# Kernel optimization log

Measured on AMD Instinct MI355X. Metric: run time of the kernel, lower is better.

Reference implementation:

```python
import jax, jax.numpy as jnp
import numpy as np

B, S, H, DIN, DOUT = 4, 2048, 8, 128, 128


def setup_inputs() -> dict:
    key = jax.random.key(0)
    ks = jax.random.split(key, 11)
    sc = 0.05
    return {
        "q": jax.random.normal(ks[0], (B, S, DIN), jnp.float32),
        "k": jax.random.normal(ks[1], (B, S, DIN), jnp.float32),
        "v": jax.random.normal(ks[2], (B, S, DOUT), jnp.float32),
        "Wq": jax.random.normal(ks[3], (DIN, DIN * H), jnp.float32) * sc,
        "bq": jax.random.normal(ks[4], (DIN * H,), jnp.float32) * sc,
        "Wk": jax.random.normal(ks[5], (DIN, DIN * H), jnp.float32) * sc,
        "bk": jax.random.normal(ks[6], (DIN * H,), jnp.float32) * sc,
        "Wv": jax.random.normal(ks[7], (DOUT, DOUT * H), jnp.float32) * sc,
        "bv": jax.random.normal(ks[8], (DOUT * H,), jnp.float32) * sc,
        "Wo": jax.random.normal(ks[9], (H * DOUT, DOUT), jnp.float32) * sc,
        "bo": jax.random.normal(ks[10], (DOUT,), jnp.float32) * sc,
    }


def reference(q, k, v, Wq, bq, Wk, bk, Wv, bv, Wo, bo):
    b, s, din = q.shape
    dout = v.shape[-1]
    h = Wq.shape[1] // din
    # project and split heads: [B, S, H, D] -> [B, H, S, D]
    qs = (q @ Wq + bq).reshape(b, s, h, din).transpose(0, 2, 1, 3)
    kh = (k @ Wk + bk).reshape(b, k.shape[1], h, din).transpose(0, 2, 1, 3)
    vh = (v @ Wv + bv).reshape(b, v.shape[1], h, dout).transpose(0, 2, 1, 3)
    # scaled dot-product attention; note the original scales by sqrt(input_dim)
    scale = 1.0 / jnp.sqrt(jnp.asarray(din, q.dtype))
    scores = jnp.einsum("bhqd,bhkd->bhqk", qs, kh) * scale
    attn = jax.nn.softmax(scores, axis=-1)
    out = jnp.einsum("bhqk,bhkd->bhqd", attn, vh)  # [B, H, S, Dout]
    out = out.transpose(0, 2, 1, 3).reshape(b, s, h * dout)
    return out @ Wo + bo
```

## Files before the change

### kernel.cpp

```cpp
#include <hip/hip_runtime.h>
#include <hip/hip_bf16.h>
#include <stdint.h>

typedef __bf16 bf16_t;
typedef bf16_t bf16x8 __attribute__((ext_vector_type(8)));
typedef bf16_t bf16x4 __attribute__((ext_vector_type(4)));
typedef float  f32x4  __attribute__((ext_vector_type(4)));

#define MFMA_BF16 __builtin_amdgcn_mfma_f32_16x16x32_bf16

constexpr int BB = 4, SS = 2048, HH = 8;
constexpr float QK_SCALE = 0.08838834764831845f;

__device__ __forceinline__ void dma16(const bf16_t* g, bf16_t* l) {
    __builtin_amdgcn_global_load_lds(
        (const __attribute__((address_space(1))) void*)g,
        (__attribute__((address_space(3))) void*)l, 16, 0, 0);
}

__global__ void prep_weights(const float* __restrict__ Wq, const float* __restrict__ Wk,
                             const float* __restrict__ Wv, const float* __restrict__ Wo,
                             bf16_t* __restrict__ WqT, bf16_t* __restrict__ WkT,
                             bf16_t* __restrict__ WvT, bf16_t* __restrict__ WoT)
{
    __shared__ float tile[64][65];
    int bid = blockIdx.x;
    int m = bid >> 5, tl = bid & 31;
    const float* src; bf16_t* dst; int R, C, tr, tc; float scale = 1.0f;
    if (m < 3) {
        src = (m == 0) ? Wq : (m == 1) ? Wk : Wv;
        dst = (m == 0) ? WqT : (m == 1) ? WkT : WvT;
        R = 128; C = 1024; tr = tl >> 4; tc = tl & 15;
        if (m == 0) scale = QK_SCALE;
    } else {
        src = Wo; dst = WoT; R = 1024; C = 128; tr = tl >> 1; tc = tl & 1;
    }
    int r0 = tr * 64, c0 = tc * 64;
    int t = threadIdx.x, rr = t >> 2, cc = (t & 3) * 16;
    const float4* s4 = (const float4*)(src + (size_t)(r0 + rr) * C + c0 + cc);
    #pragma unroll
    for (int i = 0; i < 4; ++i) {
        float4 f = s4[i];
        tile[rr][cc + 4 * i + 0] = f.x; tile[rr][cc + 4 * i + 1] = f.y;
        tile[rr][cc + 4 * i + 2] = f.z; tile[rr][cc + 4 * i + 3] = f.w;
    }
    __syncthreads();
    bf16x8 o0, o1;
    #pragma unroll
    for (int i = 0; i < 8; ++i) o0[i] = (bf16_t)(tile[cc + i][rr] * scale);
    #pragma unroll
    for (int i = 0; i < 8; ++i) o1[i] = (bf16_t)(tile[cc + 8 + i][rr] * scale);
    bf16_t* d = dst + (size_t)(c0 + rr) * R + r0 + cc;
    *(bf16x8*)d = o0;
    *(bf16x8*)(d + 8) = o1;
}

__global__ __launch_bounds__(256, 2)
void proj_kernel(const float* __restrict__ qin, const float* __restrict__ kin,
                 const float* __restrict__ vin,
                 const bf16_t* __restrict__ WqT, const bf16_t* __restrict__ WkT,
                 const bf16_t* __restrict__ WvT,
                 const float* __restrict__ bq, const float* __restrict__ bk,
                 const float* __restrict__ bv,
                 bf16_t* __restrict__ Qh, bf16_t* __restrict__ Kh, bf16_t* __restrict__ VhT)
{
    __shared__ __align__(16) bf16_t a_lds[128][136];
    __shared__ __align__(16) bf16_t b_lds[128][136];
    const int z = blockIdx.z;
    const float*  A    = (z == 0) ? qin : (z == 1) ? kin : vin;
    const bf16_t* BT   = (z == 0) ? WqT : (z == 1) ? WkT : WvT;
    const float*  bias = (z == 0) ? bq  : (z == 1) ? bk  : bv;
    bf16_t*       out  = (z == 0) ? Qh  : (z == 1) ? Kh  : VhT;
    const float   bscale = (z == 0) ? QK_SCALE : 1.0f;
    const int t  = threadIdx.x;
    const int m0 = blockIdx.x * 128;
    const int n0 = blockIdx.y * 128;
    {
        int r = t >> 1, cb = (t & 1) * 64;
        const float4* src = (const float4*)(A + (size_t)(m0 + r) * 128 + cb);
        #pragma unroll
        for (int i = 0; i < 8; ++i) {
            float4 f0 = src[2 * i], f1 = src[2 * i + 1];
            bf16x8 pk = { (bf16_t)f0.x, (bf16_t)f0.y, (bf16_t)f0.z, (bf16_t)f0.w,
                          (bf16_t)f1.x, (bf16_t)f1.y, (bf16_t)f1.z, (bf16_t)f1.w };
            *(bf16x8*)&a_lds[r][cb + 8 * i] = pk;
        }
        const bf16x8* bsrc = (const bf16x8*)(BT + (size_t)(n0 + r) * 128 + cb);
        #pragma unroll
        for (int i = 0; i < 8; ++i)
            *(bf16x8*)&b_lds[r][cb + 8 * i] = bsrc[i];
    }
    __syncthreads();
    const int w = t >> 6, lane = t & 63, q = lane >> 4, ln = lane & 15;
    const int wm = (w & 1) * 64, wn = (w >> 1) * 64;
    f32x4 acc[4][4] = {};
    if (z != 2) {
        #pragma unroll
        for (int kc = 0; kc < 4; ++kc) {
            bf16x8 af[4], bfr[4];
            #pragma unroll
            for (int mi = 0; mi < 4; ++mi)
                af[mi] = *(const bf16x8*)&a_lds[wm + mi * 16 + ln][kc * 32 + q * 8];
            #pragma unroll
            for (int ni = 0; ni < 4; ++ni)
                bfr[ni] = *(const bf16x8*)&b_lds[wn + ni * 16 + ln][kc * 32 + q * 8];
            #pragma unroll
            for (int mi = 0; mi < 4; ++mi)
                #pragma unroll
                for (int ni = 0; ni < 4; ++ni)
                    acc[mi][ni] = MFMA_BF16(af[mi], bfr[ni], acc[mi][ni], 0, 0, 0);
        }
        #pragma unroll
        for (int ni = 0; ni < 4; ++ni) {
            int col = n0 + wn + ni * 16 + ln;
            int h = col >> 7, d = col & 127;
            float bvv = bias[col] * bscale;
            #pragma unroll
            for (int mi = 0; mi < 4; ++mi) {
                int mbase = m0 + wm + mi * 16 + q * 4;
                int b = mbase >> 11, s = mbase & 2047;
                #pragma unroll
                for (int r = 0; r < 4; ++r)
                    out[((size_t)(b * HH + h) * SS + (s + r)) * 128 + d] =
                        (bf16_t)(acc[mi][ni][r] + bvv);
            }
        }
    } else {
        #pragma unroll
        for (int kc = 0; kc < 4; ++kc) {
            bf16x8 af[4], bfr[4];
            #pragma unroll
            for (int mi = 0; mi < 4; ++mi)
                af[mi] = *(const bf16x8*)&a_lds[wm + mi * 16 + ln][kc * 32 + q * 8];
            #pragma unroll
            for (int ni = 0; ni < 4; ++ni)
                bfr[ni] = *(const bf16x8*)&b_lds[wn + ni * 16 + ln][kc * 32 + q * 8];
            #pragma unroll
            for (int mi = 0; mi < 4; ++mi)
                #pragma unroll
                for (int ni = 0; ni < 4; ++ni)
                    acc[mi][ni] = MFMA_BF16(bfr[ni], af[mi], acc[mi][ni], 0, 0, 0);
        }
        #pragma unroll
        for (int ni = 0; ni < 4; ++ni) {
            #pragma unroll
            for (int r = 0; r < 4; ++r) {
                int col = n0 + wn + ni * 16 + q * 4 + r;
                int h = col >> 7, d = col & 127;
                float bvv = bias[col];
                #pragma unroll
                for (int mi = 0; mi < 4; ++mi) {
                    int mg = m0 + wm + mi * 16 + ln;
                    int b = mg >> 11, s = mg & 2047;
                    out[((size_t)(b * HH + h) * 128 + d) * SS + s] =
                        (bf16_t)(acc[mi][ni][r] + bvv);
                }
            }
        }
    }
}

__global__ __launch_bounds__(256, 2)
void attn_kernel(const bf16_t* __restrict__ Qh, const bf16_t* __restrict__ Kh,
                 const bf16_t* __restrict__ VhT, bf16_t* __restrict__ Aout)
{
    __shared__ __align__(16) bf16_t k_s[2][64 * 128];
    __shared__ __align__(16) bf16_t v_s[2][128 * 64];
    __shared__ __align__(16) bf16_t p_s[4 * 32 * 64];
    const int t = threadIdx.x;
    const int w = t >> 6, lane = t & 63, q = lane >> 4, ln = lane & 15;
    const int bh = blockIdx.y;
    const int q0 = blockIdx.x * 128;
    const size_t hb = (size_t)bh * SS * 128;

    bf16x8 qf[2][4];
    #pragma unroll
    for (int rg = 0; rg < 2; ++rg) {
        const bf16_t* qrow = Qh + hb + (size_t)(q0 + w * 32 + rg * 16 + ln) * 128;
        #pragma unroll
        for (int kc = 0; kc < 4; ++kc)
            qf[rg][kc] = *(const bf16x8*)(qrow + kc * 32 + q * 8);
    }
    const bf16_t one = (bf16_t)1.0f;
    bf16x8 ones = { one, one, one, one, one, one, one, one };
    f32x4 o[2][8] = {};
    f32x4 ol[2] = {};
    bf16_t* pw = &p_s[w * 32 * 64];

    auto stage = [&](int buf, int kv0) {
        #pragma unroll
        for (int j = 0; j < 4; ++j) {
            int row = w * 16 + j * 4 + (lane >> 4);
            int blk = (lane & 15) ^ (row & 7);
            dma16(Kh + hb + (size_t)(kv0 + row) * 128 + blk * 8,
                  &k_s[buf][(w * 16 + j * 4) * 128]);
        }
        #pragma unroll
        for (int j = 0; j < 4; ++j) {
            int row = w * 32 + j * 8 + (lane >> 3);
            int blk = (lane & 7) ^ (row & 7);
            dma16(VhT + hb + (size_t)row * SS + kv0 + blk * 8,
                  &v_s[buf][(w * 32 + j * 8) * 64]);
        }
    };

    stage(0, 0);
    for (int it = 0; it < SS / 64; ++it) {
        int cur = it & 1;
        __syncthreads();
        if (it + 1 < SS / 64) stage(cur ^ 1, (it + 1) * 64);
        const bf16_t* ks = &k_s[cur][0];
        const bf16_t* vs = &v_s[cur][0];
        f32x4 sc[2][4] = {};
        #pragma unroll
        for (int kc = 0; kc < 4; ++kc) {
            #pragma unroll
            for (int nt = 0; nt < 4; ++nt) {
                int row = nt * 16 + ln;
                bf16x8 kf = *(const bf16x8*)&ks[row * 128 + (((kc * 4 + q) ^ (ln & 7)) * 8)];
                sc[0][nt] = MFMA_BF16(kf, qf[0][kc], sc[0][nt], 0, 0, 0);
                sc[1][nt] = MFMA_BF16(kf, qf[1][kc], sc[1][nt], 0, 0, 0);
            }
        }
        #pragma unroll
        for (int rg = 0; rg < 2; ++rg) {
            #pragma unroll
            for (int nt = 0; nt < 4; ++nt) {
                bf16x4 pk;
                #pragma unroll
                for (int r = 0; r < 4; ++r)
                    pk[r] = (bf16_t)__expf(sc[rg][nt][r]);
                int row = rg * 16 + ln;
                int blk = (2 * nt + (q >> 1)) ^ (row & 7);
                *(bf16x4*)&pw[row * 64 + blk * 8 + (q & 1) * 4] = pk;
            }
        }
        #pragma unroll
        for (int c2 = 0; c2 < 2; ++c2) {
            int pblk = (c2 * 4 + q) ^ (ln & 7);
            bf16x8 pf0 = *(const bf16x8*)&pw[ln * 64 + pblk * 8];
            bf16x8 pf1 = *(const bf16x8*)&pw[(16 + ln) * 64 + pblk * 8];
            ol[0] = MFMA_BF16(pf0, ones, ol[0], 0, 0, 0);
            ol[1] = MFMA_BF16(pf1, ones, ol[1], 0, 0, 0);
            #pragma unroll
            for (int dt = 0; dt < 8; ++dt) {
                int vrow = dt * 16 + ln;
                bf16x8 vf = *(const bf16x8*)&vs[vrow * 64 + (((c2 * 4 + q) ^ (ln & 7)) * 8)];
                o[0][dt] = MFMA_BF16(pf0, vf, o[0][dt], 0, 0, 0);
                o[1][dt] = MFMA_BF16(pf1, vf, o[1][dt], 0, 0, 0);
            }
        }
    }
    const int b = bh >> 3, h = bh & 7;
    #pragma unroll
    for (int rg = 0; rg < 2; ++rg) {
        #pragma unroll
        for (int r = 0; r < 4; ++r) {
            float inv = 1.0f / ol[rg][r];
            int s = q0 + w * 32 + rg * 16 + q * 4 + r;
            bf16_t* dst = Aout + ((size_t)(b * SS + s)) * 1024 + h * 128;
            #pragma unroll
            for (int dt = 0; dt < 8; ++dt)
                dst[dt * 16 + ln] = (bf16_t)(o[rg][dt][r] * inv);
        }
    }
}

__global__ __launch_bounds__(256, 2)
void out_gemm(const bf16_t* __restrict__ A, const bf16_t* __restrict__ BT,
              float* __restrict__ part)
{
    __shared__ __align__(16) bf16_t a_s[2][32 * 64];
    __shared__ __align__(16) bf16_t b_s[2][128 * 64];
    const int t = threadIdx.x, w = t >> 6, lane = t & 63, q = lane >> 4, ln = lane & 15;
    const int m0 = blockIdx.x * 32;
    const int kbase = blockIdx.y * 512;
    const int mh = (w & 1) * 16, nh = (w >> 1) * 64;
    f32x4 acc[4] = {};

    auto stage = [&](int buf, int kk) {
        {
            int row = w * 8 + (lane >> 3);
            int blk = (lane & 7) ^ (row & 7);
            dma16(A + (size_t)(m0 + row) * 1024 + kk + blk * 8, &a_s[buf][(w * 8) * 64]);
        }
        #pragma unroll
        for (int j = 0; j < 4; ++j) {
            int row = w * 32 + j * 8 + (lane >> 3);
            int blk = (lane & 7) ^ (row & 7);
            dma16(BT + (size_t)row * 1024 + kk + blk * 8, &b_s[buf][(w * 32 + j * 8) * 64]);
        }
    };

    stage(0, kbase);
    for (int kb = 0; kb < 8; ++kb) {
        __syncthreads();
        if (kb < 7) stage((kb + 1) & 1, kbase + (kb + 1) * 64);
        const bf16_t* as = a_s[kb & 1];
        const bf16_t* bs = b_s[kb & 1];
        #pragma unroll
        for (int kc = 0; kc < 2; ++kc) {
            int arow = mh + ln;
            bf16x8 af = *(const bf16x8*)&as[arow * 64 + (((kc * 4 + q) ^ (arow & 7)) * 8)];
            #pragma unroll
            for (int ni = 0; ni < 4; ++ni) {
                int brow = nh + ni * 16 + ln;
                bf16x8 bfr = *(const bf16x8*)&bs[brow * 64 + (((kc * 4 + q) ^ (brow & 7)) * 8)];
                acc[ni] = MFMA_BF16(af, bfr, acc[ni], 0, 0, 0);
            }
        }
    }
    float* dst = part + (size_t)blockIdx.y * 8192 * 128;
    #pragma unroll
    for (int ni = 0; ni < 4; ++ni) {
        int col = nh + ni * 16 + ln;
        #pragma unroll
        for (int r = 0; r < 4; ++r)
            dst[(size_t)(m0 + mh + q * 4 + r) * 128 + col] = acc[ni][r];
    }
}

__global__ void reduce_out(const float* __restrict__ p0, const float* __restrict__ p1,
                           const float* __restrict__ bias, float* __restrict__ out)
{
    int i = (blockIdx.x * 256 + threadIdx.x) * 4;
    f32x4 a = *(const f32x4*)(p0 + i);
    f32x4 b = *(const f32x4*)(p1 + i);
    f32x4 c = *(const f32x4*)(bias + (i & 127));
    *(f32x4*)(out + i) = a + b + c;
}

extern "C" void kernel_launch(void* const* d_in, const int* in_sizes, int n_in,
                              void* d_out, int out_size, void* d_ws, size_t ws_size,
                              hipStream_t stream)
{
    const float* q  = (const float*)d_in[0];
    const float* k  = (const float*)d_in[1];
    const float* v  = (const float*)d_in[2];
    const float* Wq = (const float*)d_in[3];
    const float* bq = (const float*)d_in[4];
    const float* Wk = (const float*)d_in[5];
    const float* bk = (const float*)d_in[6];
    const float* Wv = (const float*)d_in[7];
    const float* bv = (const float*)d_in[8];
    const float* Wo = (const float*)d_in[9];
    const float* bo = (const float*)d_in[10];
    float* out = (float*)d_out;

    char* ws = (char*)d_ws;
    bf16_t* WqT  = (bf16_t*)(ws + 0 * (1 << 18));
    bf16_t* WkT  = (bf16_t*)(ws + 1 * (1 << 18));
    bf16_t* WvT  = (bf16_t*)(ws + 2 * (1 << 18));
    bf16_t* WoT  = (bf16_t*)(ws + 3 * (1 << 18));
    bf16_t* Qh   = (bf16_t*)(ws + (1 << 20));
    bf16_t* Kh   = (bf16_t*)(ws + (1 << 20) + 1 * (1 << 24));
    bf16_t* VhT  = (bf16_t*)(ws + (1 << 20) + 2 * (1 << 24));
    bf16_t* Aout = (bf16_t*)(ws + (1 << 20) + 3 * (1 << 24));
    float*  part = (float*)(ws + (1 << 20) + 4 * (1 << 24));

    prep_weights<<<128, 256, 0, stream>>>(Wq, Wk, Wv, Wo, WqT, WkT, WvT, WoT);
    proj_kernel<<<dim3(64, 8, 3), 256, 0, stream>>>(q, k, v, WqT, WkT, WvT,
                                                    bq, bk, bv, Qh, Kh, VhT);
    attn_kernel<<<dim3(SS / 128, BB * HH), 256, 0, stream>>>(Qh, Kh, VhT, Aout);
    out_gemm<<<dim3(256, 2), 256, 0, stream>>>(Aout, WoT, part);
    reduce_out<<<1024, 256, 0, stream>>>(part, part + (size_t)8192 * 128, bo, out);
}
```

Measured before the change: 190.4 us.

## Pre-convert inputs to bf16, DMA-pipeline projection, exp2 softmax, drop split-K reduce

Several changes land together. The prep kernel now also converts q/k/v to bf16, so the projection kernel can stream operands through a double-buffered global-to-LDS DMA with an XOR swizzle. Softmax uses exp2 with log2e folded into the Q scaling. The output GEMM no longer splits K, which removes the partial buffers and the separate reduce kernel and applies the bias directly. The cost is an extra bf16 copy of the inputs written to and read from global memory, and half as many blocks in the output GEMM.

```diff
diff --git a/kernel.cpp b/kernel.cpp
--- a/kernel.cpp
+++ b/kernel.cpp
@@ -11,6 +11,16 @@
 
 constexpr int BB = 4, SS = 2048, HH = 8;
 constexpr float QK_SCALE = 0.08838834764831845f;
+constexpr float LOG2E    = 1.4426950408889634f;
+constexpr float QSCL     = QK_SCALE * LOG2E;
+
+__device__ __forceinline__ float exp2_fast(float x) {
+#if __has_builtin(__builtin_amdgcn_exp2f)
+    return __builtin_amdgcn_exp2f(x);
+#else
+    return __expf(x * 0.6931471805599453f);
+#endif
+}
 
 __device__ __forceinline__ void dma16(const bf16_t* g, bf16_t* l) {
     __builtin_amdgcn_global_load_lds(
@@ -18,98 +28,130 @@
         (__attribute__((address_space(3))) void*)l, 16, 0, 0);
 }
 
-__global__ void prep_weights(const float* __restrict__ Wq, const float* __restrict__ Wk,
-                             const float* __restrict__ Wv, const float* __restrict__ Wo,
-                             bf16_t* __restrict__ WqT, bf16_t* __restrict__ WkT,
-                             bf16_t* __restrict__ WvT, bf16_t* __restrict__ WoT)
-{
-    __shared__ float tile[64][65];
-    int bid = blockIdx.x;
-    int m = bid >> 5, tl = bid & 31;
-    const float* src; bf16_t* dst; int R, C, tr, tc; float scale = 1.0f;
-    if (m < 3) {
-        src = (m == 0) ? Wq : (m == 1) ? Wk : Wv;
-        dst = (m == 0) ? WqT : (m == 1) ? WkT : WvT;
-        R = 128; C = 1024; tr = tl >> 4; tc = tl & 15;
-        if (m == 0) scale = QK_SCALE;
+__global__ void prep_kernel(const float* __restrict__ q, const float* __restrict__ k,
+                            const float* __restrict__ v,
+                            const float* __restrict__ Wq, const float* __restrict__ Wk,
+                            const float* __restrict__ Wv, const float* __restrict__ Wo,
+                            bf16_t* __restrict__ WqT, bf16_t* __restrict__ WkT,
+                            bf16_t* __restrict__ WvT, bf16_t* __restrict__ WoT,
+                            bf16_t* __restrict__ Abf)
+{
+    int bid = blockIdx.x, t = threadIdx.x;
+    if (bid < 128) {
+        __shared__ float tile[64][65];
+        int m = bid >> 5, tl = bid & 31;
+        const float* src; bf16_t* dst; int R, C, tr, tc; float scale = 1.0f;
+        if (m < 3) {
+            src = (m == 0) ? Wq : (m == 1) ? Wk : Wv;
+            dst = (m == 0) ? WqT : (m == 1) ? WkT : WvT;
+            R = 128; C = 1024; tr = tl >> 4; tc = tl & 15;
+            if (m == 0) scale = QSCL;
+        } else {
+            src = Wo; dst = WoT; R = 1024; C = 128; tr = tl >> 1; tc = tl & 1;
+        }
+        int r0 = tr * 64, c0 = tc * 64;
+        int rr = t >> 2, cc = (t & 3) * 16;
+        const float4* s4 = (const float4*)(src + (size_t)(r0 + rr) * C + c0 + cc);
+        #pragma unroll
+        for (int i = 0; i < 4; ++i) {
+            float4 f = s4[i];
+            tile[rr][cc + 4 * i + 0] = f.x; tile[rr][cc + 4 * i + 1] = f.y;
+            tile[rr][cc + 4 * i + 2] = f.z; tile[rr][cc + 4 * i + 3] = f.w;
+        }
+        __syncthreads();
+        bf16x8 o0, o1;
+        #pragma unroll
+        for (int i = 0; i < 8; ++i) o0[i] = (bf16_t)(tile[cc + i][rr] * scale);
+        #pragma unroll
+        for (int i = 0; i < 8; ++i) o1[i] = (bf16_t)(tile[cc + 8 + i][rr] * scale);
+        bf16_t* d = dst + (size_t)(c0 + rr) * R + r0 + cc;
+        *(bf16x8*)d = o0;
+        *(bf16x8*)(d + 8) = o1;
     } else {
-        src = Wo; dst = WoT; R = 1024; C = 128; tr = tl >> 1; tc = tl & 1;
-    }
-    int r0 = tr * 64, c0 = tc * 64;
-    int t = threadIdx.x, rr = t >> 2, cc = (t & 3) * 16;
-    const float4* s4 = (const float4*)(src + (size_t)(r0 + rr) * C + c0 + cc);
-    #pragma unroll
-    for (int i = 0; i < 4; ++i) {
-        float4 f = s4[i];
-        tile[rr][cc + 4 * i + 0] = f.x; tile[rr][cc + 4 * i + 1] = f.y;
-        tile[rr][cc + 4 * i + 2] = f.z; tile[rr][cc + 4 * i + 3] = f.w;
-    }
-    __syncthreads();
-    bf16x8 o0, o1;
-    #pragma unroll
-    for (int i = 0; i < 8; ++i) o0[i] = (bf16_t)(tile[cc + i][rr] * scale);
-    #pragma unroll
-    for (int i = 0; i < 8; ++i) o1[i] = (bf16_t)(tile[cc + 8 + i][rr] * scale);
-    bf16_t* d = dst + (size_t)(c0 + rr) * R + r0 + cc;
-    *(bf16x8*)d = o0;
-    *(bf16x8*)(d + 8) = o1;
+        int bid2 = bid - 128;
+        size_t base = (size_t)bid2 * 4096 + t * 16;
+        int z = (int)(base >> 20);
+        size_t off = base & 1048575;
+        const float* s = (z == 0) ? q : (z == 1) ? k : v;
+        const float4* s4 = (const float4*)(s + off);
+        bf16_t* d = Abf + (size_t)z * 1048576 + off;
+        float4 f0 = s4[0], f1 = s4[1], f2 = s4[2], f3 = s4[3];
+        bf16x8 p0 = { (bf16_t)f0.x, (bf16_t)f0.y, (bf16_t)f0.z, (bf16_t)f0.w,
+                      (bf16_t)f1.x, (bf16_t)f1.y, (bf16_t)f1.z, (bf16_t)f1.w };
+        bf16x8 p1 = { (bf16_t)f2.x, (bf16_t)f2.y, (bf16_t)f2.z, (bf16_t)f2.w,
+                      (bf16_t)f3.x, (bf16_t)f3.y, (bf16_t)f3.z, (bf16_t)f3.w };
+        *(bf16x8*)d = p0;
+        *(bf16x8*)(d + 8) = p1;
+    }
 }
 
 __global__ __launch_bounds__(256, 2)
-void proj_kernel(const float* __restrict__ qin, const float* __restrict__ kin,
-                 const float* __restrict__ vin,
+void proj_kernel(const bf16_t* __restrict__ Abf,
                  const bf16_t* __restrict__ WqT, const bf16_t* __restrict__ WkT,
                  const bf16_t* __restrict__ WvT,
                  const float* __restrict__ bq, const float* __restrict__ bk,
                  const float* __restrict__ bv,
                  bf16_t* __restrict__ Qh, bf16_t* __restrict__ Kh, bf16_t* __restrict__ VhT)
 {
-    __shared__ __align__(16) bf16_t a_lds[128][136];
-    __shared__ __align__(16) bf16_t b_lds[128][136];
+    __shared__ __align__(16) bf16_t a_s[2][128 * 64];
+    __shared__ __align__(16) bf16_t b_s[2][128 * 64];
     const int z = blockIdx.z;
-    const float*  A    = (z == 0) ? qin : (z == 1) ? kin : vin;
+    const bf16_t* A    = Abf + (size_t)z * 1048576;
     const bf16_t* BT   = (z == 0) ? WqT : (z == 1) ? WkT : WvT;
     const float*  bias = (z == 0) ? bq  : (z == 1) ? bk  : bv;
-    bf16_t*       out  = (z == 0) ? Qh  : (z == 1) ? Kh  : VhT;
-    const float   bscale = (z == 0) ? QK_SCALE : 1.0f;
-    const int t  = threadIdx.x;
+    const float   bscale = (z == 0) ? QSCL : 1.0f;
+    const int t = threadIdx.x, w = t >> 6, lane = t & 63, q = lane >> 4, ln = lane & 15;
     const int m0 = blockIdx.x * 128;
     const int n0 = blockIdx.y * 128;
-    {
-        int r = t >> 1, cb = (t & 1) * 64;
-        const float4* src = (const float4*)(A + (size_t)(m0 + r) * 128 + cb);
-        #pragma unroll
-        for (int i = 0; i < 8; ++i) {
-            float4 f0 = src[2 * i], f1 = src[2 * i + 1];
-            bf16x8 pk = { (bf16_t)f0.x, (bf16_t)f0.y, (bf16_t)f0.z, (bf16_t)f0.w,
-                          (bf16_t)f1.x, (bf16_t)f1.y, (bf16_t)f1.z, (bf16_t)f1.w };
-            *(bf16x8*)&a_lds[r][cb + 8 * i] = pk;
-        }
-        const bf16x8* bsrc = (const bf16x8*)(BT + (size_t)(n0 + r) * 128 + cb);
-        #pragma unroll
-        for (int i = 0; i < 8; ++i)
-            *(bf16x8*)&b_lds[r][cb + 8 * i] = bsrc[i];
-    }
+    const int wm = (w & 1) * 64, wn = (w >> 1) * 64;
+
+    auto stage = [&](int buf, int kb) {
+        #pragma unroll
+        for (int j = 0; j < 4; ++j) {
+            int row = w * 32 + j * 8 + (lane >> 3);
+            int u = (lane & 7) ^ (row & 7);
+            dma16(A + (size_t)(m0 + row) * 128 + kb * 64 + u * 8,
+                  &a_s[buf][(w * 32 + j * 8) * 64]);
+            dma16(BT + (size_t)(n0 + row) * 128 + kb * 64 + u * 8,
+                  &b_s[buf][(w * 32 + j * 8) * 64]);
+        }
+    };
+
+    f32x4 acc[4][4] = {};
+    stage(0, 0);
     __syncthreads();
-    const int w = t >> 6, lane = t & 63, q = lane >> 4, ln = lane & 15;
-    const int wm = (w & 1) * 64, wn = (w >> 1) * 64;
-    f32x4 acc[4][4] = {};
+    stage(1, 1);
+    #pragma unroll
+    for (int kb = 0; kb < 2; ++kb) {
+        if (kb == 1) __syncthreads();
+        const bf16_t* as = a_s[kb];
+        const bf16_t* bs = b_s[kb];
+        #pragma unroll
+        for (int kc = 0; kc < 2; ++kc) {
+            bf16x8 af[4], bfr[4];
+            #pragma unroll
+            for (int mi = 0; mi < 4; ++mi)
+                af[mi] = *(const bf16x8*)&as[(wm + mi * 16 + ln) * 64 + (((kc * 4 + q) ^ (ln & 7)) * 8)];
+            #pragma unroll
+            for (int ni = 0; ni < 4; ++ni)
+                bfr[ni] = *(const bf16x8*)&bs[(wn + ni * 16 + ln) * 64 + (((kc * 4 + q) ^ (ln & 7)) * 8)];
+            if (z != 2) {
+                #pragma unroll
+                for (int mi = 0; mi < 4; ++mi)
+                    #pragma unroll
+                    for (int ni = 0; ni < 4; ++ni)
+                        acc[mi][ni] = MFMA_BF16(af[mi], bfr[ni], acc[mi][ni], 0, 0, 0);
+            } else {
+                #pragma unroll
+                for (int mi = 0; mi < 4; ++mi)
+                    #pragma unroll
+                    for (int ni = 0; ni < 4; ++ni)
+                        acc[mi][ni] = MFMA_BF16(bfr[ni], af[mi], acc[mi][ni], 0, 0, 0);
+            }
+        }
+    }
+    bf16_t* out = (z == 0) ? Qh : (z == 1) ? Kh : VhT;
     if (z != 2) {
-        #pragma unroll
-        for (int kc = 0; kc < 4; ++kc) {
-            bf16x8 af[4], bfr[4];
-            #pragma unroll
-            for (int mi = 0; mi < 4; ++mi)
-                af[mi] = *(const bf16x8*)&a_lds[wm + mi * 16 + ln][kc * 32 + q * 8];
-            #pragma unroll
-            for (int ni = 0; ni < 4; ++ni)
-                bfr[ni] = *(const bf16x8*)&b_lds[wn + ni * 16 + ln][kc * 32 + q * 8];
-            #pragma unroll
-            for (int mi = 0; mi < 4; ++mi)
-                #pragma unroll
-                for (int ni = 0; ni < 4; ++ni)
-                    acc[mi][ni] = MFMA_BF16(af[mi], bfr[ni], acc[mi][ni], 0, 0, 0);
-        }
         #pragma unroll
         for (int ni = 0; ni < 4; ++ni) {
             int col = n0 + wn + ni * 16 + ln;
@@ -126,21 +168,6 @@
             }
         }
     } else {
-        #pragma unroll
-        for (int kc = 0; kc < 4; ++kc) {
-            bf16x8 af[4], bfr[4];
-            #pragma unroll
-            for (int mi = 0; mi < 4; ++mi)
-                af[mi] = *(const bf16x8*)&a_lds[wm + mi * 16 + ln][kc * 32 + q * 8];
-            #pragma unroll
-            for (int ni = 0; ni < 4; ++ni)
-                bfr[ni] = *(const bf16x8*)&b_lds[wn + ni * 16 + ln][kc * 32 + q * 8];
-            #pragma unroll
-            for (int mi = 0; mi < 4; ++mi)
-                #pragma unroll
-                for (int ni = 0; ni < 4; ++ni)
-                    acc[mi][ni] = MFMA_BF16(bfr[ni], af[mi], acc[mi][ni], 0, 0, 0);
-        }
         #pragma unroll
         for (int ni = 0; ni < 4; ++ni) {
             #pragma unroll
@@ -229,7 +256,7 @@
                 bf16x4 pk;
                 #pragma unroll
                 for (int r = 0; r < 4; ++r)
-                    pk[r] = (bf16_t)__expf(sc[rg][nt][r]);
+                    pk[r] = (bf16_t)exp2_fast(sc[rg][nt][r]);
                 int row = rg * 16 + ln;
                 int blk = (2 * nt + (q >> 1)) ^ (row & 7);
                 *(bf16x4*)&pw[row * 64 + blk * 8 + (q & 1) * 4] = pk;
@@ -268,66 +295,54 @@
 
 __global__ __launch_bounds__(256, 2)
 void out_gemm(const bf16_t* __restrict__ A, const bf16_t* __restrict__ BT,
-              float* __restrict__ part)
+              const float* __restrict__ bias, float* __restrict__ out)
 {
     __shared__ __align__(16) bf16_t a_s[2][32 * 64];
     __shared__ __align__(16) bf16_t b_s[2][128 * 64];
     const int t = threadIdx.x, w = t >> 6, lane = t & 63, q = lane >> 4, ln = lane & 15;
     const int m0 = blockIdx.x * 32;
-    const int kbase = blockIdx.y * 512;
     const int mh = (w & 1) * 16, nh = (w >> 1) * 64;
     f32x4 acc[4] = {};
 
     auto stage = [&](int buf, int kk) {
         {
             int row = w * 8 + (lane >> 3);
-            int blk = (lane & 7) ^ (row & 7);
-            dma16(A + (size_t)(m0 + row) * 1024 + kk + blk * 8, &a_s[buf][(w * 8) * 64]);
+            int u = (lane & 7) ^ (row & 7);
+            dma16(A + (size_t)(m0 + row) * 1024 + kk + u * 8, &a_s[buf][(w * 8) * 64]);
         }
         #pragma unroll
         for (int j = 0; j < 4; ++j) {
             int row = w * 32 + j * 8 + (lane >> 3);
-            int blk = (lane & 7) ^ (row & 7);
-            dma16(BT + (size_t)row * 1024 + kk + blk * 8, &b_s[buf][(w * 32 + j * 8) * 64]);
+            int u = (lane & 7) ^ (row & 7);
+            dma16(BT + (size_t)row * 1024 + kk + u * 8, &b_s[buf][(w * 32 + j * 8) * 64]);
         }
     };
 
-    stage(0, kbase);
-    for (int kb = 0; kb < 8; ++kb) {
+    stage(0, 0);
+    for (int kb = 0; kb < 16; ++kb) {
         __syncthreads();
-        if (kb < 7) stage((kb + 1) & 1, kbase + (kb + 1) * 64);
+        if (kb < 15) stage((kb + 1) & 1, (kb + 1) * 64);
         const bf16_t* as = a_s[kb & 1];
         const bf16_t* bs = b_s[kb & 1];
         #pragma unroll
         for (int kc = 0; kc < 2; ++kc) {
-            int arow = mh + ln;
-            bf16x8 af = *(const bf16x8*)&as[arow * 64 + (((kc * 4 + q) ^ (arow & 7)) * 8)];
+            bf16x8 af = *(const bf16x8*)&as[(mh + ln) * 64 + (((kc * 4 + q) ^ (ln & 7)) * 8)];
             #pragma unroll
             for (int ni = 0; ni < 4; ++ni) {
                 int brow = nh + ni * 16 + ln;
-                bf16x8 bfr = *(const bf16x8*)&bs[brow * 64 + (((kc * 4 + q) ^ (brow & 7)) * 8)];
+                bf16x8 bfr = *(const bf16x8*)&bs[brow * 64 + (((kc * 4 + q) ^ (ln & 7)) * 8)];
                 acc[ni] = MFMA_BF16(af, bfr, acc[ni], 0, 0, 0);
             }
         }
     }
-    float* dst = part + (size_t)blockIdx.y * 8192 * 128;
     #pragma unroll
     for (int ni = 0; ni < 4; ++ni) {
         int col = nh + ni * 16 + ln;
+        float bv = bias[col];
         #pragma unroll
         for (int r = 0; r < 4; ++r)
-            dst[(size_t)(m0 + mh + q * 4 + r) * 128 + col] = acc[ni][r];
-    }
-}
-
-__global__ void reduce_out(const float* __restrict__ p0, const float* __restrict__ p1,
-                           const float* __restrict__ bias, float* __restrict__ out)
-{
-    int i = (blockIdx.x * 256 + threadIdx.x) * 4;
-    f32x4 a = *(const f32x4*)(p0 + i);
-    f32x4 b = *(const f32x4*)(p1 + i);
-    f32x4 c = *(const f32x4*)(bias + (i & 127));
-    *(f32x4*)(out + i) = a + b + c;
+            out[(size_t)(m0 + mh + q * 4 + r) * 128 + col] = acc[ni][r] + bv;
+    }
 }
 
 extern "C" void kernel_launch(void* const* d_in, const int* in_sizes, int n_in,
@@ -352,16 +367,16 @@
     bf16_t* WkT  = (bf16_t*)(ws + 1 * (1 << 18));
     bf16_t* WvT  = (bf16_t*)(ws + 2 * (1 << 18));
     bf16_t* WoT  = (bf16_t*)(ws + 3 * (1 << 18));
-    bf16_t* Qh   = (bf16_t*)(ws + (1 << 20));
-    bf16_t* Kh   = (bf16_t*)(ws + (1 << 20) + 1 * (1 << 24));
-    bf16_t* VhT  = (bf16_t*)(ws + (1 << 20) + 2 * (1 << 24));
-    bf16_t* Aout = (bf16_t*)(ws + (1 << 20) + 3 * (1 << 24));
-    float*  part = (float*)(ws + (1 << 20) + 4 * (1 << 24));
-
-    prep_weights<<<128, 256, 0, stream>>>(Wq, Wk, Wv, Wo, WqT, WkT, WvT, WoT);
-    proj_kernel<<<dim3(64, 8, 3), 256, 0, stream>>>(q, k, v, WqT, WkT, WvT,
+    bf16_t* Abf  = (bf16_t*)(ws + (1 << 20));
+    bf16_t* Qh   = (bf16_t*)(ws + (1 << 23));
+    bf16_t* Kh   = (bf16_t*)(ws + (1 << 23) + 1 * (1 << 24));
+    bf16_t* VhT  = (bf16_t*)(ws + (1 << 23) + 2 * (1 << 24));
+    bf16_t* Aout = (bf16_t*)(ws + (1 << 23) + 3 * (1 << 24));
+
+    prep_kernel<<<896, 256, 0, stream>>>(q, k, v, Wq, Wk, Wv, Wo,
+                                         WqT, WkT, WvT, WoT, Abf);
+    proj_kernel<<<dim3(64, 8, 3), 256, 0, stream>>>(Abf, WqT, WkT, WvT,
                                                     bq, bk, bv, Qh, Kh, VhT);
     attn_kernel<<<dim3(SS / 128, BB * HH), 256, 0, stream>>>(Qh, Kh, VhT, Aout);
-    out_gemm<<<dim3(256, 2), 256, 0, stream>>>(Aout, WoT, part);
-    reduce_out<<<1024, 256, 0, stream>>>(part, part + (size_t)8192 * 128, bo, out);
-}
+    out_gemm<<<256, 256, 0, stream>>>(Aout, WoT, bo, out);
+}
```

Measured after the change: 185.6 us. 2.5% less time.
